# Optimization experiments

Hardware: AMD Instinct MI355X
Metric: run time of the kernel (lower is better)

The kernel has to match this reference:

```python
import jax, jax.numpy as jnp
import numpy as np

H, C = 4, 64          # heads, per-head channels
NB, NG = 30000, 6000  # bus nodes, gen nodes
EL, EG = 250000, 12000

def setup_inputs():
    ks = iter(jax.random.split(jax.random.key(0), 64))
    def nrm(shape, scale=1.0):
        return jax.random.normal(next(ks), shape, jnp.float32) * scale
    inp = {}
    inp['x_bus'] = nrm((NB, 32))
    inp['x_gen'] = nrm((NG, 16))
    inp['ea_line'] = jax.random.uniform(next(ks), (EL, 6), jnp.float32)
    inp['ea_g2b'] = jax.random.uniform(next(ks), (EG, 6), jnp.float32)
    inp['ea_b2g'] = jax.random.uniform(next(ks), (EG, 6), jnp.float32)
    inp['proj_gen_w'] = nrm((16, 32), 16 ** -0.5)
    inp['proj_gen_b'] = jnp.zeros((32,), jnp.float32)
    for l, (din, dout) in enumerate([(32, 256), (256, 256), (256, 64)]):
        sc = din ** -0.5
        inp['Wl%d' % l] = nrm((3, din, H * C), sc)
        inp['Wr%d' % l] = nrm((3, din, H * C), sc)
        inp['We%d' % l] = nrm((3, 6, H * C), 6 ** -0.5)
        inp['att%d' % l] = nrm((3, H, C), 0.1)
        inp['bc%d' % l] = jnp.zeros((3, dout), jnp.float32)
        inp['temp%d' % l] = jnp.ones((3,), jnp.float32)
        inp['lnw%d' % l] = jnp.ones((2, dout), jnp.float32)
        inp['lnb%d' % l] = jnp.zeros((2, dout), jnp.float32)
    inp['rp0_w'] = nrm((2, 32, 256), 32 ** -0.5)
    inp['rp0_b'] = jnp.zeros((2, 256), jnp.float32)
    inp['rp2_w'] = nrm((2, 256, 64), 256 ** -0.5)
    inp['rp2_b'] = jnp.zeros((2, 64), jnp.float32)
    inp['src_line'] = jax.random.randint(next(ks), (EL,), 0, NB, jnp.int32)
    inp['dst_line'] = jax.random.randint(next(ks), (EL,), 0, NB, jnp.int32)
    inp['src_g2b'] = jax.random.randint(next(ks), (EG,), 0, NG, jnp.int32)
    inp['dst_g2b'] = jax.random.randint(next(ks), (EG,), 0, NB, jnp.int32)
    inp['src_b2g'] = jax.random.randint(next(ks), (EG,), 0, NB, jnp.int32)
    inp['dst_b2g'] = jax.random.randint(next(ks), (EG,), 0, NG, jnp.int32)
    return inp

def _conv(xs, xd, src, dst, ea, Wl, Wr, We, att, bias, temp, concat, nd):
    # PhysicsGATv2Conv: overwrite last edge-attr column with physics prior tau/|Z| (physics_weight=1, z_index=3)
    ea = ea.at[:, -1].set(temp / jnp.maximum(ea[:, 3], 1e-6))
    xl = (xs @ Wl).reshape(-1, H, C)   # [Ns,H,C]
    xr = (xd @ Wr).reshape(-1, H, C)   # [Nd,H,C]
    m = xl[src] + xr[dst] + (ea @ We).reshape(-1, H, C)  # [E,H,C]
    logits = (jax.nn.leaky_relu(m, 0.2) * att).sum(-1)   # [E,H]
    mx = jax.ops.segment_max(logits, dst, num_segments=nd)
    mx = jnp.where(jnp.isfinite(mx), mx, 0.0)
    ex = jnp.exp(logits - mx[dst])
    alpha = ex / (jax.ops.segment_sum(ex, dst, num_segments=nd)[dst] + 1e-16)
    o = jax.ops.segment_sum(xl[src] * alpha[..., None], dst, num_segments=nd)  # [Nd,H,C]
    o = o.reshape(nd, H * C) if concat else o.mean(1)
    return o + bias

def _ln(x, w, b):
    mu = x.mean(-1, keepdims=True)
    v = ((x - mu) ** 2).mean(-1, keepdims=True)
    return (x - mu) / jnp.sqrt(v + 1e-5) * w + b

def _fwd(x_bus, x_gen, ea_line, ea_g2b, ea_b2g, proj_gen_w, proj_gen_b,
         Wl0, Wr0, We0, att0, bc0, temp0, lnw0, lnb0,
         Wl1, Wr1, We1, att1, bc1, temp1, lnw1, lnb1,
         Wl2, Wr2, We2, att2, bc2, temp2, lnw2, lnb2,
         rp0_w, rp0_b, rp2_w, rp2_b,
         src_line, dst_line, src_g2b, dst_g2b, src_b2g, dst_b2g):
    xb = x_bus                               # bus projector is Identity (32 == max dim)
    xg = x_gen @ proj_gen_w + proj_gen_b     # gen 16 -> 32
    layers = [(Wl0, Wr0, We0, att0, bc0, temp0, lnw0, lnb0, True),
              (Wl1, Wr1, We1, att1, bc1, temp1, lnw1, lnb1, True),
              (Wl2, Wr2, We2, att2, bc2, temp2, lnw2, lnb2, False)]
    for l, (Wl, Wr, We, att, bc, tp, lw, lb, concat) in enumerate(layers):
        rb, rg = xb, xg
        # to_hetero aggr='sum': one conv per edge type, sum into destination node type
        ob = (_conv(xb, xb, src_line, dst_line, ea_line, Wl[0], Wr[0], We[0], att[0], bc[0], tp[0], concat, NB)
              + _conv(xg, xb, src_g2b, dst_g2b, ea_g2b, Wl[1], Wr[1], We[1], att[1], bc[1], tp[1], concat, NB))
        og = _conv(xb, xg, src_b2g, dst_b2g, ea_b2g, Wl[2], Wr[2], We[2], att[2], bc[2], tp[2], concat, NG)
        xb = _ln(ob, lw[0], lb[0])
        xg = _ln(og, lw[1], lb[1])
        if l == 0:
            xb = xb + rb @ rp0_w[0] + rp0_b[0]
            xg = xg + rg @ rp0_w[1] + rp0_b[1]
        elif l == 1:
            xb = xb + rb
            xg = xg + rg
        else:
            xb = xb + rb @ rp2_w[0] + rp2_b[0]
            xg = xg + rg @ rp2_w[1] + rp2_b[1]
        if l < 2:
            xb = jax.nn.elu(xb)
            xg = jax.nn.elu(xg)
    # output_projector is Identity (final_dim == output_dim == 64); concat node-type outputs
    return jnp.concatenate([xb, xg], 0)

def reference(x_bus, x_gen, ea_line, ea_g2b, ea_b2g, proj_gen_w, proj_gen_b,
              Wl0, Wr0, We0, att0, bc0, temp0, lnw0, lnb0,
              Wl1, Wr1, We1, att1, bc1, temp1, lnw1, lnb1,
              Wl2, Wr2, We2, att2, bc2, temp2, lnw2, lnb2,
              rp0_w, rp0_b, rp2_w, rp2_b,
              src_line, dst_line, src_g2b, dst_g2b, src_b2g, dst_b2g):
    return _fwd(x_bus, x_gen, ea_line, ea_g2b, ea_b2g, proj_gen_w, proj_gen_b,
                Wl0, Wr0, We0, att0, bc0, temp0, lnw0, lnb0,
                Wl1, Wr1, We1, att1, bc1, temp1, lnw1, lnb1,
                Wl2, Wr2, We2, att2, bc2, tem2 := temp2, lnw2, lnb2,
                rp0_w, rp0_b, rp2_w, rp2_b,
                src_line, dst_line, src_g2b, dst_g2b, src_b2g, dst_b2g)
```

## Files before the change

### kernel.cpp

```cpp
#include <hip/hip_runtime.h>
#include <math.h>

#define NBUS 30000
#define NGEN 6000
#define NEL 250000
#define NEG 12000

#define AS1 __attribute__((address_space(1)))
#define AS3 __attribute__((address_space(3)))

typedef unsigned short u16;
typedef __attribute__((ext_vector_type(8))) short bf16x8;
typedef __attribute__((ext_vector_type(4))) float f32x4;

__device__ __forceinline__ u16 f2b(float x) {
  unsigned u = __float_as_uint(x);
  unsigned r = (u + 0x7FFFu + ((u >> 16) & 1u)) >> 16;
  return (u16)r;
}
__device__ __forceinline__ float b2f(u16 x) {
  return __uint_as_float((unsigned)x << 16);
}
__device__ __forceinline__ f32x4 splat4(float v) {
  f32x4 r = {v, v, v, v};
  return r;
}
__device__ __forceinline__ f32x4 b2f4(ushort4 v) {
  f32x4 r;
  r.x = b2f(v.x); r.y = b2f(v.y); r.z = b2f(v.z); r.w = b2f(v.w);
  return r;
}

__global__ void zeroi(int* __restrict__ p, int n) {
  int i = blockIdx.x * blockDim.x + threadIdx.x;
  int st = gridDim.x * blockDim.x;
  for (; i < n; i += st) p[i] = 0;
}

__global__ void cast_k(const float* __restrict__ s, u16* __restrict__ d, int n) {
  int i = blockIdx.x * 256 + threadIdx.x;
  if (i < n) d[i] = f2b(s[i]);
}

struct CsrArgs {
  const int* dst[3];
  const int* src[3];
  const float* ea[3];
  const float* tmp0;
  const float* tmp1;
  const float* tmp2;
  int* cnt[3];
  int* rowptr[3];
  int* srcC[3];
  float* eaC[3];
  int* psum[3];
  int E[3];
  int N[3];
};

__global__ void hist_b(CsrArgs a) {
  int ty = blockIdx.y;
  int i = blockIdx.x * 256 + threadIdx.x;
  if (i < a.E[ty]) atomicAdd(&a.cnt[ty][a.dst[ty][i]], 1);
}

__global__ __launch_bounds__(1024) void scan_p1(CsrArgs a) {
  int ty = blockIdx.y;
  int n = a.N[ty];
  int base = blockIdx.x * 1024;
  if (base >= n) return;
  int tid = threadIdx.x, lane = tid & 63, wv = tid >> 6;
  int i = base + tid;
  int v = (i < n) ? a.cnt[ty][i] : 0;
#pragma unroll
  for (int off = 32; off >= 1; off >>= 1) v += __shfl_xor(v, off);
  __shared__ int w[16];
  if (lane == 0) w[wv] = v;
  __syncthreads();
  if (tid < 16) {
    int t = w[tid];
#pragma unroll
    for (int off = 8; off >= 1; off >>= 1) t += __shfl_xor(t, off, 16);
    if (tid == 0) a.psum[ty][blockIdx.x] = t;
  }
}

__global__ __launch_bounds__(64) void scan_p2(CsrArgs a) {
  int ty = blockIdx.y;
  int nb = (a.N[ty] + 1023) / 1024;
  int tid = threadIdx.x;
  int v = (tid < nb) ? a.psum[ty][tid] : 0;
  int x = v;
#pragma unroll
  for (int off = 1; off < 64; off <<= 1) {
    int y = __shfl_up(x, off, 64);
    if (tid >= off) x += y;
  }
  if (tid < nb) a.psum[ty][tid] = x - v;
}

__global__ __launch_bounds__(1024) void scan_p3(CsrArgs a) {
  int ty = blockIdx.y;
  int n = a.N[ty];
  int base = blockIdx.x * 1024;
  if (base >= n) return;
  int tid = threadIdx.x, lane = tid & 63, wv = tid >> 6;
  int i = base + tid;
  int v = (i < n) ? a.cnt[ty][i] : 0;
  int x = v;
#pragma unroll
  for (int off = 1; off < 64; off <<= 1) {
    int y = __shfl_up(x, off, 64);
    if (lane >= off) x += y;
  }
  __shared__ int w[16];
  if (lane == 63) w[wv] = x;
  __syncthreads();
  if (tid < 16) {
    int t = w[tid];
#pragma unroll
    for (int off = 1; off < 16; off <<= 1) {
      int y = __shfl_up(t, off, 16);
      if (tid >= off) t += y;
    }
    w[tid] = t;
  }
  __syncthreads();
  int woff = (wv == 0) ? 0 : w[wv - 1];
  int incl = a.psum[ty][blockIdx.x] + woff + x;
  if (i < n) {
    a.rowptr[ty][i + 1] = incl;
    a.cnt[ty][i] = incl - v;
  }
  if (i == 0) a.rowptr[ty][0] = 0;
}

__global__ void scatter_b(CsrArgs a) {
  int ty = blockIdx.y;
  int i = blockIdx.x * 256 + threadIdx.x;
  if (i >= a.E[ty]) return;
  int p = atomicAdd(&a.cnt[ty][a.dst[ty][i]], 1);
  a.srcC[ty][p] = a.src[ty][i];
  const float* s = a.ea[ty] + (size_t)i * 6;
  float e3 = s[3];
  float inv = 1.f / fmaxf(e3, 1e-6f);
  float4 r0 = make_float4(s[0], s[1], s[2], e3);
  float4 r1 = make_float4(s[4], a.tmp0[ty] * inv, a.tmp1[ty] * inv,
                          a.tmp2[ty] * inv);
  float* d = a.eaC[ty] + (size_t)p * 8;
  *(float4*)d = r0;
  *(float4*)(d + 4) = r1;
}

__global__ void gen_proj(const float* __restrict__ x, const float* __restrict__ w,
                         const float* __restrict__ b, u16* __restrict__ o16) {
  int idx = blockIdx.x * blockDim.x + threadIdx.x;
  if (idx >= NGEN * 32) return;
  int i = idx >> 5, c = idx & 31;
  float acc = b[c];
#pragma unroll
  for (int k = 0; k < 16; ++k) acc += x[i * 16 + k] * w[k * 32 + c];
  o16[idx] = f2b(acc);
}

struct PackArgs {
  const float* src[24];
  int off[24];
  int lgN[24];
  int total[24];
  int K[24];
};
__global__ void pack_multi(PackArgs a, u16* __restrict__ Wt) {
  int j = blockIdx.y;
  int idx = blockIdx.x * 256 + threadIdx.x;
  if (idx >= a.total[j]) return;
  int N1 = (1 << a.lgN[j]) - 1;
  int n = idx & N1;
  int k = idx >> a.lgN[j];
  Wt[(size_t)a.off[j] + (size_t)n * a.K[j] + k] = f2b(a.src[j][idx]);
}

__global__ __launch_bounds__(256) void gemm_both(
    const u16* __restrict__ Ab, const u16* __restrict__ Ag,
    const u16* __restrict__ Wt, int goff,
    u16* __restrict__ Cb, u16* __restrict__ Cg,
    int K, int Nb, int Ng, int ybus)
{
  __shared__ __align__(16) u16 As[128 * 32];
  __shared__ __align__(16) u16 Bs[128 * 32];
  const int t = threadIdx.x;
  const int w = t >> 6, lane = t & 63;
  const u16* A; const u16* W; u16* C; int M, Ncols, bn;
  if ((int)blockIdx.y < ybus) {
    A = Ab; W = Wt; C = Cb; M = NBUS; Ncols = Nb; bn = blockIdx.y * 128;
  } else {
    A = Ag; W = Wt + goff; C = Cg; M = NGEN; Ncols = Ng; bn = (blockIdx.y - ybus) * 128;
  }
  const int bm = blockIdx.x * 128;
  if (bm >= M) return;
  const int wm = (w & 1) * 64, wn = (w >> 1) * 64;
  const int lr = lane & 15, q = lane >> 4;
  const int srow = lane >> 2;
  const int blk = (lane & 3) ^ (srow & 3);
  f32x4 acc[4][4] = {};
  for (int k0 = 0; k0 < K; k0 += 32) {
#pragma unroll
    for (int sseg = 0; sseg < 2; ++sseg) {
      int seg = w + (sseg << 2);
      int row = (seg << 4) + srow;
      int ga = bm + row; if (ga > M - 1) ga = M - 1;
      const u16* gpa = A + (size_t)ga * K + k0 + (blk << 3);
      __builtin_amdgcn_global_load_lds((AS1 void*)gpa, (AS3 void*)(As + (seg << 9)),
                                       16, 0, 0);
      int gb = bn + row;
      const u16* gpb = W + (size_t)gb * K + k0 + (blk << 3);
      __builtin_amdgcn_global_load_lds((AS1 void*)gpb, (AS3 void*)(Bs + (seg << 9)),
                                       16, 0, 0);
    }
    __syncthreads();
    bf16x8 af[4], bg[4];
#pragma unroll
    for (int i = 0; i < 4; ++i) {
      int r = wm + i * 16 + lr;
      af[i] = *(const bf16x8*)&As[(r << 5) + ((q ^ (r & 3)) << 3)];
    }
#pragma unroll
    for (int j = 0; j < 4; ++j) {
      int r = wn + j * 16 + lr;
      bg[j] = *(const bf16x8*)&Bs[(r << 5) + ((q ^ (r & 3)) << 3)];
    }
#pragma unroll
    for (int i = 0; i < 4; ++i)
#pragma unroll
      for (int j = 0; j < 4; ++j)
        acc[i][j] = __builtin_amdgcn_mfma_f32_16x16x32_bf16(
            af[i], bg[j], acc[i][j], 0, 0, 0);
    __syncthreads();
  }
#pragma unroll
  for (int i = 0; i < 4; ++i) {
    int row0 = bm + wm + i * 16 + q * 4;
#pragma unroll
    for (int j = 0; j < 4; ++j) {
      int col = bn + wn + j * 16 + lr;
      if (col < Ncols) {
#pragma unroll
        for (int r = 0; r < 4; ++r) {
          int row = row0 + r;
          if (row < M) C[(size_t)row * Ncols + col] = f2b(acc[i][j][r]);
        }
      }
    }
  }
}


#define CS_F1(lv, ev, fv, idx) do { \
    int rc_ = (idx) < nch ? (idx) : nch - 1; \
    int s_ = __builtin_amdgcn_readlane(vsrc, rc_); \
    lv = *(const ushort4*)(xl + (size_t)(unsigned)(s_ * ldl + ch)); \
    const float* ep_ = ebase + (unsigned)(rc_ * 8); \
    ev = *(const float4*)ep_; \
    fv = *(const float4*)(ep_ + 4); \
  } while (0)

#define CS_FETCH(S, base) do { \
    CS_F1(l##S##0, e##S##0, f##S##0, (base)); \
    CS_F1(l##S##1, e##S##1, f##S##1, (base) + 1); \
  } while (0)

#define CS_EDGE(xv, ev, fv, pv) do { \
    f32x4 m_ = xv + rx; \
    m_ = __builtin_elementwise_fma(splat4(ev.x), w0, m_); \
    m_ = __builtin_elementwise_fma(splat4(ev.y), w1, m_); \
    m_ = __builtin_elementwise_fma(splat4(ev.z), w2, m_); \
    m_ = __builtin_elementwise_fma(splat4(ev.w), w3, m_); \
    m_ = __builtin_elementwise_fma(splat4(fv.x), w4, m_); \
    float t_ = (TS == 1) ? fv.y : (TS == 2) ? fv.z : fv.w; \
    m_ = __builtin_elementwise_fma(splat4(t_), w5, m_); \
    m_ = __builtin_elementwise_max(m_, m_ * 0.2f); \
    pv = m_.x * av.x; \
    pv = fmaf(m_.y, av.y, pv); \
    pv = fmaf(m_.z, av.z, pv); \
    pv = fmaf(m_.w, av.w, pv); \
  } while (0)

#define CS_COMPUTE(S, base) do { \
    f32x4 x0_ = b2f4(l##S##0), x1_ = b2f4(l##S##1); \
    float p0_, p1_; \
    CS_EDGE(x0_, e##S##0, f##S##0, p0_); \
    CS_EDGE(x1_, e##S##1, f##S##1, p1_); \
    p0_ += __shfl_xor(p0_, 1); p0_ += __shfl_xor(p0_, 2); \
    p0_ += __shfl_xor(p0_, 4); p0_ += __shfl_xor(p0_, 8); \
    p1_ += __shfl_xor(p1_, 1); p1_ += __shfl_xor(p1_, 2); \
    p1_ += __shfl_xor(p1_, 4); p1_ += __shfl_xor(p1_, 8); \
    if ((base) >= nch) p0_ = -INFINITY; \
    if ((base) + 1 >= nch) p1_ = -INFINITY; \
    float nm_ = fmaxf(mx, fmaxf(p0_, p1_)); \
    float sc_ = __expf(mx - nm_); \
    float q0_ = __expf(p0_ - nm_), q1_ = __expf(p1_ - nm_); \
    mx = nm_; \
    den = den * sc_ + (q0_ + q1_); \
    acc = acc * splat4(sc_); \
    acc = __builtin_elementwise_fma(splat4(q0_), x0_, acc); \
    acc = __builtin_elementwise_fma(splat4(q1_), x1_, acc); \
  } while (0)

template<int TS>
__device__ __forceinline__ f32x4 conv_set(
    int node, int beg, int end, int ch,
    const int* __restrict__ srcc, const float* __restrict__ eac,
    const u16* __restrict__ xl, int ldl,
    const u16* __restrict__ xr, int ldr,
    const float* __restrict__ We, const float* __restrict__ att)
{
  f32x4 w0 = *(const f32x4*)(We + ch);
  f32x4 w1 = *(const f32x4*)(We + 256 + ch);
  f32x4 w2 = *(const f32x4*)(We + 512 + ch);
  f32x4 w3 = *(const f32x4*)(We + 768 + ch);
  f32x4 w4 = *(const f32x4*)(We + 1024 + ch);
  f32x4 w5 = *(const f32x4*)(We + 1280 + ch);
  f32x4 av = *(const f32x4*)(att + ch);
  f32x4 rx = b2f4(*(const ushort4*)(xr + (size_t)(unsigned)(node * ldr + ch)));
  float mx = -INFINITY, den = 0.f;
  f32x4 acc = {0.f, 0.f, 0.f, 0.f};
  int lane = ch >> 2;

  for (int cb = beg; cb < end; cb += 64) {
    int nch = end - cb;
    if (nch > 64) nch = 64;
    nch = __builtin_amdgcn_readfirstlane(nch);
    int cbu = __builtin_amdgcn_readfirstlane(cb);
    const float* ebase = eac + (size_t)(unsigned)cbu * 8u;
    int li = lane < nch ? lane : nch - 1;
    int vsrc = srcc[cb + li];
    int np = (nch + 1) >> 1;

    ushort4 la0, la1, lb0, lb1;
    float4 ea0, ea1, eb0, eb1;
    float4 fa0, fa1, fb0, fb1;

    CS_FETCH(a, 0);
    int g = 0;
    for (; g + 2 < np; g += 2) {
      CS_FETCH(b, (g + 1) << 1);
      CS_COMPUTE(a, g << 1);
      CS_FETCH(a, (g + 2) << 1);
      CS_COMPUTE(b, (g + 1) << 1);
    }
    if (g + 1 < np) {
      CS_FETCH(b, (g + 1) << 1);
      CS_COMPUTE(a, g << 1);
      CS_COMPUTE(b, (g + 1) << 1);
    } else {
      CS_COMPUTE(a, g << 1);
    }
  }
  float inv = 1.f / (den + 1e-16f);
  return acc * splat4(inv);
}

struct ConvP {
  const int* __restrict__ rpA; const int* __restrict__ srcA;
  const float* __restrict__ eaA;
  const u16* __restrict__ xlA; const u16* __restrict__ xrA;
  const float* __restrict__ WeA; const float* __restrict__ attA;
  const int* __restrict__ rpB; const int* __restrict__ srcB;
  const float* __restrict__ eaB;
  const u16* __restrict__ xlB; const u16* __restrict__ xrB;
  const float* __restrict__ WeB; const float* __restrict__ attB;
  const float* __restrict__ b1; const float* __restrict__ b2;
  const float* __restrict__ lnw; const float* __restrict__ lnb;
  const u16* __restrict__ res16;
  float* __restrict__ outf; u16* __restrict__ out16;
  int ldlA, ldrA, ldlB, ldrB, ld16, N;
};

template<int MODE, int TS>
__global__ __launch_bounds__(256) void conv_fused(ConvP bus, ConvP gen, int nbBus) {
  const bool isb = (int)blockIdx.x < nbBus;
#define SEL(f) (isb ? bus.f : gen.f)
  const int* __restrict__ rpA = SEL(rpA);
  const int* __restrict__ srcA = SEL(srcA);
  const float* __restrict__ eaA = SEL(eaA);
  const u16* __restrict__ xlA = SEL(xlA);
  const u16* __restrict__ xrA = SEL(xrA);
  const float* __restrict__ WeA = SEL(WeA);
  const float* __restrict__ attA = SEL(attA);
  const int* __restrict__ rpB = SEL(rpB);
  const int N = SEL(N);
  const int ldlA = SEL(ldlA), ldrA = SEL(ldrA);

  const int wv = threadIdx.x >> 6;
  const int lane = threadIdx.x & 63;
  const int ch = lane << 2;
  const int wid = (isb ? (int)blockIdx.x : (int)blockIdx.x - nbBus) * 4 + wv;
  const int nw = (isb ? nbBus : (int)gridDim.x - nbBus) * 4;

#pragma clang loop unroll(disable)
  for (int node = wid; node < N; node += nw) {
    int begA = rpA[node], endA = rpA[node + 1];
    int begB = 0, endB = 0;
    if (rpB) { begB = rpB[node]; endB = rpB[node + 1]; }
    f32x4 o = conv_set<TS>(node, begA, endA, ch, srcA, eaA, xlA, ldlA,
                           xrA, ldrA, WeA, attA);
    if (rpB && begB < endB) {
      f32x4 ob = conv_set<TS>(node, begB, endB, ch, SEL(srcB), SEL(eaB),
                              SEL(xlB), SEL(ldlB), SEL(xrB), SEL(ldrB),
                              SEL(WeB), SEL(attB));
      o[0] += ob[0]; o[1] += ob[1]; o[2] += ob[2]; o[3] += ob[3];
    }
    const float* __restrict__ b1 = SEL(b1);
    const float* __restrict__ b2 = SEL(b2);
    const float* __restrict__ lnw = SEL(lnw);
    const float* __restrict__ lnb = SEL(lnb);
    const u16* __restrict__ res16 = SEL(res16);
    const int ld16 = SEL(ld16);
    if (MODE == 0) {
      int c = ch;
      float4 bb = *(const float4*)(b1 + c);
      float v0 = o[0] + bb.x, v1 = o[1] + bb.y, v2 = o[2] + bb.z, v3 = o[3] + bb.w;
      if (b2) {
        float4 b2v = *(const float4*)(b2 + c);
        v0 += b2v.x; v1 += b2v.y; v2 += b2v.z; v3 += b2v.w;
      }
      float s = v0 + v1 + v2 + v3;
#pragma unroll
      for (int m = 32; m >= 1; m >>= 1) s += __shfl_xor(s, m);
      float mu = s * (1.f / 256.f);
      float d0 = v0 - mu, d1 = v1 - mu, d2 = v2 - mu, d3 = v3 - mu;
      float q = d0*d0 + d1*d1 + d2*d2 + d3*d3;
#pragma unroll
      for (int m = 32; m >= 1; m >>= 1) q += __shfl_xor(q, m);
      float rs = rsqrtf(q * (1.f / 256.f) + 1e-5f);
      float4 lw = *(const float4*)(lnw + c);
      float4 lb = *(const float4*)(lnb + c);
      float y0 = d0 * rs * lw.x + lb.x;
      float y1 = d1 * rs * lw.y + lb.y;
      float y2 = d2 * rs * lw.z + lb.z;
      float y3 = d3 * rs * lw.w + lb.w;
      ushort4 r = *(const ushort4*)(res16 + (size_t)node * ld16 + c);
      y0 += b2f(r.x); y1 += b2f(r.y); y2 += b2f(r.z); y3 += b2f(r.w);
      y0 = (y0 > 0.f) ? y0 : expm1f(y0);
      y1 = (y1 > 0.f) ? y1 : expm1f(y1);
      y2 = (y2 > 0.f) ? y2 : expm1f(y2);
      y3 = (y3 > 0.f) ? y3 : expm1f(y3);
      ushort4 o16;
      o16.x = f2b(y0); o16.y = f2b(y1); o16.z = f2b(y2); o16.w = f2b(y3);
      u16* __restrict__ out16 = SEL(out16);
      *(ushort4*)(out16 + (size_t)node * 256 + c) = o16;
    } else {
      float h0 = o[0], h1 = o[1], h2 = o[2], h3 = o[3];
      h0 += __shfl_xor(h0, 16); h0 += __shfl_xor(h0, 32);
      h1 += __shfl_xor(h1, 16); h1 += __shfl_xor(h1, 32);
      h2 += __shfl_xor(h2, 16); h2 += __shfl_xor(h2, 32);
      h3 += __shfl_xor(h3, 16); h3 += __shfl_xor(h3, 32);
      int cc = (lane & 15) << 2;
      float4 bb = *(const float4*)(b1 + cc);
      float v0 = 0.25f * h0 + bb.x, v1 = 0.25f * h1 + bb.y;
      float v2 = 0.25f * h2 + bb.z, v3 = 0.25f * h3 + bb.w;
      if (b2) {
        float4 b2v = *(const float4*)(b2 + cc);
        v0 += b2v.x; v1 += b2v.y; v2 += b2v.z; v3 += b2v.w;
      }
      float s = v0 + v1 + v2 + v3;
#pragma unroll
      for (int m = 8; m >= 1; m >>= 1) s += __shfl_xor(s, m);
      float mu = s * (1.f / 64.f);
      float d0 = v0 - mu, d1 = v1 - mu, d2 = v2 - mu, d3 = v3 - mu;
      float q = d0*d0 + d1*d1 + d2*d2 + d3*d3;
#pragma unroll
      for (int m = 8; m >= 1; m >>= 1) q += __shfl_xor(q, m);
      float rs = rsqrtf(q * (1.f / 64.f) + 1e-5f);
      float4 lw = *(const float4*)(lnw + cc);
      float4 lb = *(const float4*)(lnb + cc);
      ushort4 r = *(const ushort4*)(res16 + (size_t)node * ld16 + cc);
      float y0 = d0 * rs * lw.x + lb.x + b2f(r.x);
      float y1 = d1 * rs * lw.y + lb.y + b2f(r.y);
      float y2 = d2 * rs * lw.z + lb.z + b2f(r.z);
      float y3 = d3 * rs * lw.w + lb.w + b2f(r.w);
      float* __restrict__ outf = SEL(outf);
      if (lane < 16)
        *(float4*)(outf + (size_t)node * 64 + cc) = make_float4(y0, y1, y2, y3);
    }
  }
#undef SEL
}

extern "C" void kernel_launch(void* const* d_in, const int* in_sizes, int n_in,
                              void* d_out, int out_size, void* d_ws, size_t ws_size,
                              hipStream_t stream) {
  const float* x_bus = (const float*)d_in[0];
  const float* x_gen = (const float*)d_in[1];
  const float* ea[3] = {(const float*)d_in[2], (const float*)d_in[3], (const float*)d_in[4]};
  const float* pw = (const float*)d_in[5];
  const float* pb = (const float*)d_in[6];
  const float* Wl[3] = {(const float*)d_in[7], (const float*)d_in[15], (const float*)d_in[23]};
  const float* Wr[3] = {(const float*)d_in[8], (const float*)d_in[16], (const float*)d_in[24]};
  const float* We[3] = {(const float*)d_in[9], (const float*)d_in[17], (const float*)d_in[25]};
  const float* att[3] = {(const float*)d_in[10], (const float*)d_in[18], (const float*)d_in[26]};
  const float* bc[3] = {(const float*)d_in[11], (const float*)d_in[19], (const float*)d_in[27]};
  const float* temp[3] = {(const float*)d_in[12], (const float*)d_in[20], (const float*)d_in[28]};
  const float* lnw[3] = {(const float*)d_in[13], (const float*)d_in[21], (const float*)d_in[29]};
  const float* lnb[3] = {(const float*)d_in[14], (const float*)d_in[22], (const float*)d_in[30]};
  const float* rp0_w = (const float*)d_in[31];
  const float* rp2_w = (const float*)d_in[33];
  const int* srcs[3] = {(const int*)d_in[35], (const int*)d_in[37], (const int*)d_in[39]};
  const int* dsts[3] = {(const int*)d_in[36], (const int*)d_in[38], (const int*)d_in[40]};

  float* ws = (float*)d_ws;
  size_t off = 0;
  auto alloc = [&](size_t n) { float* p = ws + off; off += n; return p; };
  u16* xb16_0 = (u16*)alloc((size_t)NBUS * 16);
  u16* xg16_0 = (u16*)alloc((size_t)NGEN * 16);
  u16* xb16 = (u16*)alloc((size_t)NBUS * 128);
  u16* xg16 = (u16*)alloc((size_t)NGEN * 128);
  u16* Pbus = (u16*)alloc((size_t)NBUS * 640);
  u16* Pgen = (u16*)alloc((size_t)NGEN * 384);
  u16* Wt = (u16*)alloc((size_t)886000 / 2);
  float* eaC0 = alloc((size_t)NEL * 8);
  float* eaC1 = alloc((size_t)NEG * 8);
  float* eaC2 = alloc((size_t)NEG * 8);
  int* cw_all = (int*)alloc(NBUS + NBUS + NGEN);
  int* rp_line = (int*)alloc(NBUS + 1);
  int* rp_g2b = (int*)alloc(NBUS + 1);
  int* rp_b2g = (int*)alloc(NGEN + 1);
  int* sc_line = (int*)alloc(NEL);
  int* sc_g2b = (int*)alloc(NEG);
  int* sc_b2g = (int*)alloc(NEG);
  int* psum = (int*)alloc(3 * 32);
  (void)ws_size; (void)in_sizes; (void)n_in; (void)out_size;

  CsrArgs ca;
  for (int t = 0; t < 3; ++t) { ca.dst[t] = dsts[t]; ca.src[t] = srcs[t]; ca.ea[t] = ea[t]; }
  ca.tmp0 = temp[0]; ca.tmp1 = temp[1]; ca.tmp2 = temp[2];
  ca.cnt[0] = cw_all; ca.cnt[1] = cw_all + NBUS; ca.cnt[2] = cw_all + 2 * NBUS;
  ca.rowptr[0] = rp_line; ca.rowptr[1] = rp_g2b; ca.rowptr[2] = rp_b2g;
  ca.srcC[0] = sc_line; ca.srcC[1] = sc_g2b; ca.srcC[2] = sc_b2g;
  ca.eaC[0] = eaC0; ca.eaC[1] = eaC1; ca.eaC[2] = eaC2;
  ca.psum[0] = psum; ca.psum[1] = psum + 32; ca.psum[2] = psum + 64;
  ca.E[0] = NEL; ca.E[1] = NEG; ca.E[2] = NEG;
  ca.N[0] = NBUS; ca.N[1] = NBUS; ca.N[2] = NGEN;

  int egrid = (NEL + 255) / 256;
  hipLaunchKernelGGL(zeroi, dim3(64), dim3(1024), 0, stream, cw_all, 2 * NBUS + NGEN);
  hipLaunchKernelGGL(hist_b, dim3(egrid, 3), dim3(256), 0, stream, ca);
  hipLaunchKernelGGL(scan_p1, dim3(30, 3), dim3(1024), 0, stream, ca);
  hipLaunchKernelGGL(scan_p2, dim3(1, 3), dim3(64), 0, stream, ca);
  hipLaunchKernelGGL(scan_p3, dim3(30, 3), dim3(1024), 0, stream, ca);
  hipLaunchKernelGGL(scatter_b, dim3(egrid, 3), dim3(256), 0, stream, ca);

  hipLaunchKernelGGL(gen_proj, dim3((NGEN * 32 + 255) / 256), dim3(256), 0, stream,
                     x_gen, pw, pb, xg16_0);
  hipLaunchKernelGGL(cast_k, dim3((NBUS * 32 + 255) / 256), dim3(256), 0, stream,
                     x_bus, xb16_0, NBUS * 32);

  const int K_l[3] = {32, 256, 256};
  const int Nbus_l[3] = {1280, 1024, 1088};
  const int Ngen_l[3] = {768, 512, 576};
  int Lbase[3], goff_l[3];
  {
    int b = 0;
    for (int l = 0; l < 3; ++l) {
      Lbase[l] = b;
      goff_l[l] = Nbus_l[l] * K_l[l];
      b += (Nbus_l[l] + Ngen_l[l]) * K_l[l];
    }
  }
  PackArgs pa = {};
  int ns = 0;
  auto add = [&](const float* src, int offel, int N_, int lg, int K) {
    pa.src[ns] = src; pa.off[ns] = offel; pa.lgN[ns] = lg;
    pa.total[ns] = K * N_; pa.K[ns] = K; ++ns;
  };
  for (int l = 0; l < 3; ++l) {
    int K = K_l[l];
    size_t sl = (size_t)K * 256;
    int L = Lbase[l], go = goff_l[l];
    add(Wl[l], L, 256, 8, K);
    add(Wr[l], L + 256 * K, 256, 8, K);
    add(Wr[l] + sl, L + 512 * K, 256, 8, K);
    add(Wl[l] + 2 * sl, L + 768 * K, 256, 8, K);
    add(Wl[l] + sl, L + go, 256, 8, K);
    add(Wr[l] + 2 * sl, L + go + 256 * K, 256, 8, K);
    if (l == 0) {
      add(rp0_w, L + 1024 * K, 256, 8, K);
      add(rp0_w + 32 * 256, L + go + 512 * K, 256, 8, K);
    } else if (l == 2) {
      add(rp2_w, L + 1024 * K, 64, 6, K);
      add(rp2_w + 256 * 64, L + go + 512 * K, 64, 6, K);
    }
  }
  hipLaunchKernelGGL(pack_multi, dim3(256, ns), dim3(256), 0, stream, pa, Wt);

  const int nbBus = 1792;
  const int nbGen = 256;

  for (int l = 0; l < 3; ++l) {
    const int K = K_l[l];
    const int Nb = Nbus_l[l], Ng = Ngen_l[l];
    const u16* Ab = (l == 0) ? xb16_0 : xb16;
    const u16* Ag = (l == 0) ? xg16_0 : xg16;

    int ybus = (Nb + 127) / 128, ygen = (Ng + 127) / 128;
    hipLaunchKernelGGL(gemm_both, dim3((NBUS + 127) / 128, ybus + ygen),
                       dim3(256), 0, stream,
                       Ab, Ag, Wt + Lbase[l], goff_l[l], Pbus, Pgen, K, Nb, Ng, ybus);

    ConvP pb_ = {};
    pb_.rpA = rp_line; pb_.srcA = sc_line; pb_.eaA = eaC0;
    pb_.xlA = Pbus; pb_.ldlA = Nb; pb_.xrA = Pbus + 256; pb_.ldrA = Nb;
    pb_.WeA = We[l]; pb_.attA = att[l];
    pb_.rpB = rp_g2b; pb_.srcB = sc_g2b; pb_.eaB = eaC1;
    pb_.xlB = Pgen; pb_.ldlB = Ng; pb_.xrB = Pbus + 512; pb_.ldrB = Nb;
    pb_.WeB = We[l] + 1536; pb_.attB = att[l] + 256;
    pb_.N = NBUS;
    ConvP pg_ = {};
    pg_.rpA = rp_b2g; pg_.srcA = sc_b2g; pg_.eaA = eaC2;
    pg_.xlA = Pbus + 768; pg_.ldlA = Nb; pg_.xrA = Pgen + 256; pg_.ldrA = Ng;
    pg_.WeA = We[l] + 3072; pg_.attA = att[l] + 512;
    pg_.rpB = nullptr;
    pg_.N = NGEN;
    dim3 gall(nbBus + nbGen), blk(256);

    if (l < 2) {
      pb_.b1 = bc[l]; pb_.b2 = bc[l] + 256; pb_.lnw = lnw[l]; pb_.lnb = lnb[l];
      pg_.b1 = bc[l] + 512; pg_.b2 = nullptr;
      pg_.lnw = lnw[l] + 256; pg_.lnb = lnb[l] + 256;
      if (l == 0) {
        pb_.res16 = Pbus + 1024; pb_.ld16 = Nb;
        pg_.res16 = Pgen + 512; pg_.ld16 = Ng;
      } else {
        pb_.res16 = xb16; pb_.ld16 = 256;
        pg_.res16 = xg16; pg_.ld16 = 256;
      }
      pb_.outf = nullptr; pb_.out16 = xb16;
      pg_.outf = nullptr; pg_.out16 = xg16;
      if (l == 0)
        hipLaunchKernelGGL((conv_fused<0, 1>), gall, blk, 0, stream, pb_, pg_, nbBus);
      else
        hipLaunchKernelGGL((conv_fused<0, 2>), gall, blk, 0, stream, pb_, pg_, nbBus);
    } else {
      pb_.b1 = bc[2]; pb_.b2 = bc[2] + 64; pb_.lnw = lnw[2]; pb_.lnb = lnb[2];
      pb_.res16 = Pbus + 1024; pb_.ld16 = Nb;
      pb_.outf = (float*)d_out; pb_.out16 = nullptr;
      pg_.b1 = bc[2] + 128; pg_.b2 = nullptr; pg_.lnw = lnw[2] + 64; pg_.lnb = lnb[2] + 64;
      pg_.res16 = Pgen + 512; pg_.ld16 = Ng;
      pg_.outf = (float*)d_out + (size_t)NBUS * 64; pg_.out16 = nullptr;
      hipLaunchKernelGGL((conv_fused<1, 3>), gall, blk, 0, stream, pb_, pg_, nbBus);
    }
  }
}
```

Before: 540.6 us.

## Stage GEMM epilogue through LDS, use one wave per node, fast ELU exp

```diff
diff --git a/kernel.cpp b/kernel.cpp
--- a/kernel.cpp
+++ b/kernel.cpp
@@ -188,6 +188,7 @@
 {
   __shared__ __align__(16) u16 As[128 * 32];
   __shared__ __align__(16) u16 Bs[128 * 32];
+  __shared__ __align__(16) u16 Cs[32 * 128];
   const int t = threadIdx.x;
   const int w = t >> 6, lane = t & 63;
   const u16* A; const u16* W; u16* C; int M, Ncols, bn;
@@ -239,17 +240,24 @@
   }
 #pragma unroll
   for (int i = 0; i < 4; ++i) {
-    int row0 = bm + wm + i * 16 + q * 4;
-#pragma unroll
-    for (int j = 0; j < 4; ++j) {
-      int col = bn + wn + j * 16 + lr;
-      if (col < Ncols) {
-#pragma unroll
-        for (int r = 0; r < 4; ++r) {
-          int row = row0 + r;
-          if (row < M) C[(size_t)row * Ncols + col] = f2b(acc[i][j][r]);
-        }
-      }
+    __syncthreads();
+    int lrow = (wm >> 2) + q * 4;
+#pragma unroll
+    for (int j = 0; j < 4; ++j)
+#pragma unroll
+      for (int r = 0; r < 4; ++r)
+        Cs[(lrow + r) * 128 + wn + j * 16 + lr] = f2b(acc[i][j][r]);
+    __syncthreads();
+#pragma unroll
+    for (int it = 0; it < 2; ++it) {
+      int chunk = t + it * 256;
+      int row = chunk >> 4;
+      int cg = (chunk & 15) * 8;
+      int grow = bm + ((row & 16) ? 64 : 0) + i * 16 + (row & 15);
+      int gcol = bn + cg;
+      if (grow < M && gcol < Ncols)
+        *(bf16x8*)&C[(size_t)grow * Ncols + gcol] =
+            *(const bf16x8*)&Cs[row * 128 + cg];
     }
   }
 }
@@ -379,6 +387,7 @@
 template<int MODE, int TS>
 __global__ __launch_bounds__(256) void conv_fused(ConvP bus, ConvP gen, int nbBus) {
   const bool isb = (int)blockIdx.x < nbBus;
+  const int grp = isb ? blockIdx.x : blockIdx.x - nbBus;
 #define SEL(f) (isb ? bus.f : gen.f)
   const int* __restrict__ rpA = SEL(rpA);
   const int* __restrict__ srcA = SEL(srcA);
@@ -391,98 +400,93 @@
   const int N = SEL(N);
   const int ldlA = SEL(ldlA), ldrA = SEL(ldrA);
 
-  const int wv = threadIdx.x >> 6;
-  const int lane = threadIdx.x & 63;
-  const int ch = lane << 2;
-  const int wid = (isb ? (int)blockIdx.x : (int)blockIdx.x - nbBus) * 4 + wv;
-  const int nw = (isb ? nbBus : (int)gridDim.x - nbBus) * 4;
-
-#pragma clang loop unroll(disable)
-  for (int node = wid; node < N; node += nw) {
-    int begA = rpA[node], endA = rpA[node + 1];
-    int begB = 0, endB = 0;
-    if (rpB) { begB = rpB[node]; endB = rpB[node + 1]; }
-    f32x4 o = conv_set<TS>(node, begA, endA, ch, srcA, eaA, xlA, ldlA,
-                           xrA, ldrA, WeA, attA);
-    if (rpB && begB < endB) {
-      f32x4 ob = conv_set<TS>(node, begB, endB, ch, SEL(srcB), SEL(eaB),
-                              SEL(xlB), SEL(ldlB), SEL(xrB), SEL(ldrB),
-                              SEL(WeB), SEL(attB));
-      o[0] += ob[0]; o[1] += ob[1]; o[2] += ob[2]; o[3] += ob[3];
-    }
-    const float* __restrict__ b1 = SEL(b1);
-    const float* __restrict__ b2 = SEL(b2);
-    const float* __restrict__ lnw = SEL(lnw);
-    const float* __restrict__ lnb = SEL(lnb);
-    const u16* __restrict__ res16 = SEL(res16);
-    const int ld16 = SEL(ld16);
-    if (MODE == 0) {
-      int c = ch;
-      float4 bb = *(const float4*)(b1 + c);
-      float v0 = o[0] + bb.x, v1 = o[1] + bb.y, v2 = o[2] + bb.z, v3 = o[3] + bb.w;
-      if (b2) {
-        float4 b2v = *(const float4*)(b2 + c);
-        v0 += b2v.x; v1 += b2v.y; v2 += b2v.z; v3 += b2v.w;
-      }
-      float s = v0 + v1 + v2 + v3;
-#pragma unroll
-      for (int m = 32; m >= 1; m >>= 1) s += __shfl_xor(s, m);
-      float mu = s * (1.f / 256.f);
-      float d0 = v0 - mu, d1 = v1 - mu, d2 = v2 - mu, d3 = v3 - mu;
-      float q = d0*d0 + d1*d1 + d2*d2 + d3*d3;
-#pragma unroll
-      for (int m = 32; m >= 1; m >>= 1) q += __shfl_xor(q, m);
-      float rs = rsqrtf(q * (1.f / 256.f) + 1e-5f);
-      float4 lw = *(const float4*)(lnw + c);
-      float4 lb = *(const float4*)(lnb + c);
-      float y0 = d0 * rs * lw.x + lb.x;
-      float y1 = d1 * rs * lw.y + lb.y;
-      float y2 = d2 * rs * lw.z + lb.z;
-      float y3 = d3 * rs * lw.w + lb.w;
-      ushort4 r = *(const ushort4*)(res16 + (size_t)node * ld16 + c);
-      y0 += b2f(r.x); y1 += b2f(r.y); y2 += b2f(r.z); y3 += b2f(r.w);
-      y0 = (y0 > 0.f) ? y0 : expm1f(y0);
-      y1 = (y1 > 0.f) ? y1 : expm1f(y1);
-      y2 = (y2 > 0.f) ? y2 : expm1f(y2);
-      y3 = (y3 > 0.f) ? y3 : expm1f(y3);
-      ushort4 o16;
-      o16.x = f2b(y0); o16.y = f2b(y1); o16.z = f2b(y2); o16.w = f2b(y3);
-      u16* __restrict__ out16 = SEL(out16);
-      *(ushort4*)(out16 + (size_t)node * 256 + c) = o16;
-    } else {
-      float h0 = o[0], h1 = o[1], h2 = o[2], h3 = o[3];
-      h0 += __shfl_xor(h0, 16); h0 += __shfl_xor(h0, 32);
-      h1 += __shfl_xor(h1, 16); h1 += __shfl_xor(h1, 32);
-      h2 += __shfl_xor(h2, 16); h2 += __shfl_xor(h2, 32);
-      h3 += __shfl_xor(h3, 16); h3 += __shfl_xor(h3, 32);
-      int cc = (lane & 15) << 2;
-      float4 bb = *(const float4*)(b1 + cc);
-      float v0 = 0.25f * h0 + bb.x, v1 = 0.25f * h1 + bb.y;
-      float v2 = 0.25f * h2 + bb.z, v3 = 0.25f * h3 + bb.w;
-      if (b2) {
-        float4 b2v = *(const float4*)(b2 + cc);
-        v0 += b2v.x; v1 += b2v.y; v2 += b2v.z; v3 += b2v.w;
-      }
-      float s = v0 + v1 + v2 + v3;
-#pragma unroll
-      for (int m = 8; m >= 1; m >>= 1) s += __shfl_xor(s, m);
-      float mu = s * (1.f / 64.f);
-      float d0 = v0 - mu, d1 = v1 - mu, d2 = v2 - mu, d3 = v3 - mu;
-      float q = d0*d0 + d1*d1 + d2*d2 + d3*d3;
-#pragma unroll
-      for (int m = 8; m >= 1; m >>= 1) q += __shfl_xor(q, m);
-      float rs = rsqrtf(q * (1.f / 64.f) + 1e-5f);
-      float4 lw = *(const float4*)(lnw + cc);
-      float4 lb = *(const float4*)(lnb + cc);
-      ushort4 r = *(const ushort4*)(res16 + (size_t)node * ld16 + cc);
-      float y0 = d0 * rs * lw.x + lb.x + b2f(r.x);
-      float y1 = d1 * rs * lw.y + lb.y + b2f(r.y);
-      float y2 = d2 * rs * lw.z + lb.z + b2f(r.z);
-      float y3 = d3 * rs * lw.w + lb.w + b2f(r.w);
-      float* __restrict__ outf = SEL(outf);
-      if (lane < 16)
-        *(float4*)(outf + (size_t)node * 64 + cc) = make_float4(y0, y1, y2, y3);
-    }
+  int node = grp * 4 + (threadIdx.x >> 6);
+  int lane = threadIdx.x & 63;
+  if (node >= N) return;
+  int ch = lane << 2;
+  int begA = rpA[node], endA = rpA[node + 1];
+  int begB = 0, endB = 0;
+  if (rpB) { begB = rpB[node]; endB = rpB[node + 1]; }
+  f32x4 o = conv_set<TS>(node, begA, endA, ch, srcA, eaA, xlA, ldlA,
+                         xrA, ldrA, WeA, attA);
+  if (rpB && begB < endB) {
+    f32x4 ob = conv_set<TS>(node, begB, endB, ch, SEL(srcB), SEL(eaB),
+                            SEL(xlB), SEL(ldlB), SEL(xrB), SEL(ldrB),
+                            SEL(WeB), SEL(attB));
+    o[0] += ob[0]; o[1] += ob[1]; o[2] += ob[2]; o[3] += ob[3];
+  }
+  const float* __restrict__ b1 = SEL(b1);
+  const float* __restrict__ b2 = SEL(b2);
+  const float* __restrict__ lnw = SEL(lnw);
+  const float* __restrict__ lnb = SEL(lnb);
+  const u16* __restrict__ res16 = SEL(res16);
+  const int ld16 = SEL(ld16);
+  if (MODE == 0) {
+    int c = ch;
+    float4 bb = *(const float4*)(b1 + c);
+    float v0 = o[0] + bb.x, v1 = o[1] + bb.y, v2 = o[2] + bb.z, v3 = o[3] + bb.w;
+    if (b2) {
+      float4 b2v = *(const float4*)(b2 + c);
+      v0 += b2v.x; v1 += b2v.y; v2 += b2v.z; v3 += b2v.w;
+    }
+    float s = v0 + v1 + v2 + v3;
+#pragma unroll
+    for (int m = 32; m >= 1; m >>= 1) s += __shfl_xor(s, m);
+    float mu = s * (1.f / 256.f);
+    float d0 = v0 - mu, d1 = v1 - mu, d2 = v2 - mu, d3 = v3 - mu;
+    float q = d0*d0 + d1*d1 + d2*d2 + d3*d3;
+#pragma unroll
+    for (int m = 32; m >= 1; m >>= 1) q += __shfl_xor(q, m);
+    float rs = rsqrtf(q * (1.f / 256.f) + 1e-5f);
+    float4 lw = *(const float4*)(lnw + c);
+    float4 lb = *(const float4*)(lnb + c);
+    float y0 = d0 * rs * lw.x + lb.x;
+    float y1 = d1 * rs * lw.y + lb.y;
+    float y2 = d2 * rs * lw.z + lb.z;
+    float y3 = d3 * rs * lw.w + lb.w;
+    ushort4 r = *(const ushort4*)(res16 + (size_t)node * ld16 + c);
+    y0 += b2f(r.x); y1 += b2f(r.y); y2 += b2f(r.z); y3 += b2f(r.w);
+    y0 = (y0 > 0.f) ? y0 : __expf(y0) - 1.f;
+    y1 = (y1 > 0.f) ? y1 : __expf(y1) - 1.f;
+    y2 = (y2 > 0.f) ? y2 : __expf(y2) - 1.f;
+    y3 = (y3 > 0.f) ? y3 : __expf(y3) - 1.f;
+    ushort4 o16;
+    o16.x = f2b(y0); o16.y = f2b(y1); o16.z = f2b(y2); o16.w = f2b(y3);
+    u16* __restrict__ out16 = SEL(out16);
+    *(ushort4*)(out16 + (size_t)node * 256 + c) = o16;
+  } else {
+    float h0 = o[0], h1 = o[1], h2 = o[2], h3 = o[3];
+    h0 += __shfl_xor(h0, 16); h0 += __shfl_xor(h0, 32);
+    h1 += __shfl_xor(h1, 16); h1 += __shfl_xor(h1, 32);
+    h2 += __shfl_xor(h2, 16); h2 += __shfl_xor(h2, 32);
+    h3 += __shfl_xor(h3, 16); h3 += __shfl_xor(h3, 32);
+    int cc = (lane & 15) << 2;
+    float4 bb = *(const float4*)(b1 + cc);
+    float v0 = 0.25f * h0 + bb.x, v1 = 0.25f * h1 + bb.y;
+    float v2 = 0.25f * h2 + bb.z, v3 = 0.25f * h3 + bb.w;
+    if (b2) {
+      float4 b2v = *(const float4*)(b2 + cc);
+      v0 += b2v.x; v1 += b2v.y; v2 += b2v.z; v3 += b2v.w;
+    }
+    float s = v0 + v1 + v2 + v3;
+#pragma unroll
+    for (int m = 8; m >= 1; m >>= 1) s += __shfl_xor(s, m);
+    float mu = s * (1.f / 64.f);
+    float d0 = v0 - mu, d1 = v1 - mu, d2 = v2 - mu, d3 = v3 - mu;
+    float q = d0*d0 + d1*d1 + d2*d2 + d3*d3;
+#pragma unroll
+    for (int m = 8; m >= 1; m >>= 1) q += __shfl_xor(q, m);
+    float rs = rsqrtf(q * (1.f / 64.f) + 1e-5f);
+    float4 lw = *(const float4*)(lnw + cc);
+    float4 lb = *(const float4*)(lnb + cc);
+    ushort4 r = *(const ushort4*)(res16 + (size_t)node * ld16 + cc);
+    float y0 = d0 * rs * lw.x + lb.x + b2f(r.x);
+    float y1 = d1 * rs * lw.y + lb.y + b2f(r.y);
+    float y2 = d2 * rs * lw.z + lb.z + b2f(r.z);
+    float y3 = d3 * rs * lw.w + lb.w + b2f(r.w);
+    float* __restrict__ outf = SEL(outf);
+    if (lane < 16)
+      *(float4*)(outf + (size_t)node * 64 + cc) = make_float4(y0, y1, y2, y3);
   }
 #undef SEL
 }
@@ -593,8 +597,8 @@
   }
   hipLaunchKernelGGL(pack_multi, dim3(256, ns), dim3(256), 0, stream, pa, Wt);
 
-  const int nbBus = 1792;
-  const int nbGen = 256;
+  const int nbBus = (NBUS + 3) / 4;
+  const int nbGen = (NGEN + 3) / 4;
 
   for (int l = 0; l < 3; ++l) {
     const int K = K_l[l];
```

Measured after the change: 476.7 us. 1.13x faster.
